# Kernel optimization log

Measured on AMD Instinct MI355X. Metric: run time of the kernel, lower is better.

Reference implementation:

```python
import jax, jax.numpy as jnp
import numpy as np

DIM = 64
NUM_GRAPHS = 256
SLOPE = 11.0 / 48.0  # RReLU eval slope = ((1/8)+(1/3))/2
EPS = 1e-5


def _bn(x, g, b):
    m = x.mean(0)
    v = x.var(0)  # biased, matches torch BN normalization
    return (x - m) * jax.lax.rsqrt(v + EPS) * g + b


def _rrelu(x):
    return jnp.where(x >= 0, x, SLOPE * x)


def _gru(x, h, Wih, Whh, bih, bhh):
    gi = x @ Wih.T + bih
    gh = h @ Whh.T + bhh
    ir, iz, inn = jnp.split(gi, 3, -1)
    hr, hz, hn = jnp.split(gh, 3, -1)
    r = jax.nn.sigmoid(ir + hr)
    z = jax.nn.sigmoid(iz + hz)
    n = jnp.tanh(inn + r * hn)
    return (1.0 - z) * n + z * h


def _nnconv(x, ei, We, bias, n_nodes):
    # edge-conditioned conv: gather src, per-edge matmul, scatter-mean to dst
    src, dst = ei[0], ei[1]
    msg = jnp.einsum('ei,eio->eo', x[src], We)
    s = jax.ops.segment_sum(msg, dst, num_segments=n_nodes)
    cnt = jax.ops.segment_sum(jnp.ones((ei.shape[1],), x.dtype), dst, num_segments=n_nodes)
    return s / jnp.maximum(cnt, 1.0)[:, None] + bias


def _seg_softmax(e, seg, nseg):
    m = jax.ops.segment_max(e, seg, num_segments=nseg)
    ex = jnp.exp(e - m[seg])
    den = jax.ops.segment_sum(ex, seg, num_segments=nseg)
    return ex / den[seg]


def _set2set(x, seg, nseg, Wih, Whh, bih, bhh, steps=3):
    H = x.shape[-1]
    q_star = jnp.zeros((nseg, 2 * H), x.dtype)
    h = jnp.zeros((nseg, H), x.dtype)
    c = jnp.zeros((nseg, H), x.dtype)
    for _ in range(steps):
        gates = q_star @ Wih.T + bih + h @ Whh.T + bhh
        i, f, g, o = jnp.split(gates, 4, -1)
        c = jax.nn.sigmoid(f) * c + jax.nn.sigmoid(i) * jnp.tanh(g)
        h = jax.nn.sigmoid(o) * jnp.tanh(c)
        e = jnp.sum(x * h[seg], -1)
        a = _seg_softmax(e, seg, nseg)
        r = jax.ops.segment_sum(a[:, None] * x, seg, num_segments=nseg)
        q_star = jnp.concatenate([h, r], -1)
    return q_star


def reference(x, edge_index, edge_attr, edge_index3, edge_attr3, batch,
              bnx_g, bnx_b, Wn, bnode, We, be, Wnn1, bias1,
              Wih1, Whh1, bih1, bhh1, bnc_g, bnc_b, Wc1, bc1, Wc2, bc2,
              Wnn2, bias2, Wih2, Whh2, bih2, bhh2,
              Ws_ih, Ws_hh, bs_ih, bs_hh, bno_g, bno_b, Ww, Wb):
    N = x.shape[0]
    out = _rrelu(_bn(x, bnx_g, bnx_b) @ Wn + bnode)          # [N, 64]
    ea = _rrelu(edge_attr @ We + be)                          # [E, 12]
    W1 = (ea @ Wnn1).reshape(-1, DIM, DIM)                    # [E, 64, 64]
    h = out
    for _ in range(2):
        m = _rrelu(_nnconv(out, edge_index, W1, bias1, N))
        h = _gru(m, h, Wih1, Whh1, bih1, bhh1)
        out = h
    out = _bn(out, bnc_g, bnc_b)
    out = _rrelu(out @ Wc1 + bc1)
    out = _rrelu(out @ Wc2 + bc2)                             # [N, 128] (dropout=identity in eval)
    ei3s = jnp.concatenate([edge_index3, edge_index3[::-1]], axis=1)
    ea3s = jnp.concatenate([edge_attr3, edge_attr3], axis=0)
    W2 = (ea3s @ Wnn2).reshape(-1, 2 * DIM, 2 * DIM)          # [2*E3, 128, 128]
    h = out
    for _ in range(2):
        m = _rrelu(_nnconv(out, ei3s, W2, bias2, N))
        h = _gru(m, h, Wih2, Whh2, bih2, bhh2)
        out = h
    cbi = batch[edge_index3[0]]
    pool = _set2set(out, batch, NUM_GRAPHS, Ws_ih, Ws_hh, bs_ih, bs_hh)[cbi]
    t0 = out[edge_index3[0]]
    t1 = out[edge_index3[1]]
    yhat = jnp.concatenate([(t0 + t1) * 0.5, t0 * t1, (t0 - t1) ** 2, pool], axis=1)  # [E3, 640]
    yhat = _bn(yhat, bno_g, bno_b)
    w = edge_attr3 @ Ww
    b = edge_attr3 @ Wb
    return jnp.sum(yhat * w, axis=1) + b[:, 0]


def setup_inputs() -> dict:
    key = jax.random.key(0)
    ks = iter(jax.random.split(key, 64))
    def nrm(shape, scale=1.0):
        return jax.random.normal(next(ks), shape, jnp.float32) * scale
    def lin(i, o):
        return nrm((i, o), 1.0 / np.sqrt(i))
    N, E, E3 = 8192, 16384, 1024
    inp = {}
    inp['x'] = nrm((N, 8))
    inp['edge_index'] = jax.random.randint(next(ks), (2, E), 0, N)
    inp['edge_attr'] = nrm((E, 19))
    inp['edge_index3'] = jax.random.randint(next(ks), (2, E3), 0, N)
    inp['edge_attr3'] = nrm((E3, 8))
    inp['batch'] = jnp.repeat(jnp.arange(NUM_GRAPHS), N // NUM_GRAPHS)
    inp['bnx_g'] = jnp.ones(8); inp['bnx_b'] = jnp.zeros(8)
    inp['Wn'] = lin(8, 64); inp['bnode'] = jnp.zeros(64)
    inp['We'] = lin(19, 12); inp['be'] = jnp.zeros(12)
    inp['Wnn1'] = lin(12, DIM * DIM) * 0.5; inp['bias1'] = jnp.zeros(64)
    inp['Wih1'] = nrm((192, 64), 1.0 / np.sqrt(64)); inp['Whh1'] = nrm((192, 64), 1.0 / np.sqrt(64))
    inp['bih1'] = jnp.zeros(192); inp['bhh1'] = jnp.zeros(192)
    inp['bnc_g'] = jnp.ones(64); inp['bnc_b'] = jnp.zeros(64)
    inp['Wc1'] = lin(64, 128); inp['bc1'] = jnp.zeros(128)
    inp['Wc2'] = lin(128, 128); inp['bc2'] = jnp.zeros(128)
    inp['Wnn2'] = lin(8, 4 * DIM * DIM) * 0.5; inp['bias2'] = jnp.zeros(128)
    inp['Wih2'] = nrm((384, 128), 1.0 / np.sqrt(128)); inp['Whh2'] = nrm((384, 128), 1.0 / np.sqrt(128))
    inp['bih2'] = jnp.zeros(384); inp['bhh2'] = jnp.zeros(384)
    inp['Ws_ih'] = nrm((512, 256), 1.0 / np.sqrt(256)); inp['Ws_hh'] = nrm((512, 128), 1.0 / np.sqrt(128))
    inp['bs_ih'] = jnp.zeros(512); inp['bs_hh'] = jnp.zeros(512)
    inp['bno_g'] = jnp.ones(640); inp['bno_b'] = jnp.zeros(640)
    inp['Ww'] = lin(8, 640); inp['Wb'] = lin(8, 1)
    return inp
```

## Files before the change

kernel.cpp:

```cpp
#include <hip/hip_runtime.h>
#include <hip/hip_bf16.h>
#include <math.h>

#define N_NODES 8192
#define N_EDGES 16384
#define N_E3    1024
#define NGRAPH  256
#define NPG     32
#define SLOPE   (11.0f/48.0f)
#define BN_EPS  1e-5f

__device__ __forceinline__ float rrelu(float v){ return v >= 0.f ? v : SLOPE*v; }
__device__ __forceinline__ float sigm(float v){ return 1.f/(1.f+__expf(-v)); }

typedef _Float16 f16;
typedef __attribute__((ext_vector_type(8))) _Float16 half8v;
typedef __attribute__((ext_vector_type(4))) float f32x4;

template<int PRE, int ACT>
__device__ __forceinline__ void mgemm_body(
    const float* __restrict__ A, const f16* __restrict__ Wh,
    const float* __restrict__ bias,
    const float* __restrict__ q0, const float* __restrict__ q1,
    const float* __restrict__ q2, const float* __restrict__ q3,
    const int* __restrict__ rowidx,
    float* __restrict__ C, int M, int K, int J, int blk) {
  int t = threadIdx.x;
  int lane = t & 63, wv = t >> 6;
  int jt = J >> 6;
  int bm = blk / jt, bj = blk % jt;
  int n0 = (bm << 6) + (wv << 4);
  int j0 = bj << 6;
  int row = n0 + (lane & 15);
  int arow = rowidx ? rowidx[row] : row;
  int kb0 = (lane >> 4) * 8;

  f32x4 acc[4] = {{0.f,0.f,0.f,0.f},{0.f,0.f,0.f,0.f},{0.f,0.f,0.f,0.f},{0.f,0.f,0.f,0.f}};

  float pre_dn = 1.f;
  if (PRE == 1) pre_dn = 1.f / fmaxf(q0[row], 1.f);

  for (int k0 = 0; k0 < K; k0 += 32) {
    int kb = k0 + kb0;
    const float* ap = A + (size_t)arow * K + kb;
    float4 v0 = *(const float4*)ap;
    float4 v1 = *(const float4*)(ap + 4);
    if (PRE == 1) {
      float4 b0 = *(const float4*)(q1 + kb);
      float4 b1 = *(const float4*)(q1 + kb + 4);
      v0.x = rrelu(v0.x*pre_dn + b0.x); v0.y = rrelu(v0.y*pre_dn + b0.y);
      v0.z = rrelu(v0.z*pre_dn + b0.z); v0.w = rrelu(v0.w*pre_dn + b0.w);
      v1.x = rrelu(v1.x*pre_dn + b1.x); v1.y = rrelu(v1.y*pre_dn + b1.y);
      v1.z = rrelu(v1.z*pre_dn + b1.z); v1.w = rrelu(v1.w*pre_dn + b1.w);
    } else if (PRE == 2) {
      float4 m0 = *(const float4*)(q0 + kb), m1 = *(const float4*)(q0 + kb + 4);
      float4 s0 = *(const float4*)(q1 + kb), s1 = *(const float4*)(q1 + kb + 4);
      float4 g0 = *(const float4*)(q2 + kb), g1 = *(const float4*)(q2 + kb + 4);
      float4 h0 = *(const float4*)(q3 + kb), h1 = *(const float4*)(q3 + kb + 4);
      v0.x = (v0.x-m0.x)*rsqrtf(s0.x+BN_EPS)*g0.x + h0.x;
      v0.y = (v0.y-m0.y)*rsqrtf(s0.y+BN_EPS)*g0.y + h0.y;
      v0.z = (v0.z-m0.z)*rsqrtf(s0.z+BN_EPS)*g0.z + h0.z;
      v0.w = (v0.w-m0.w)*rsqrtf(s0.w+BN_EPS)*g0.w + h0.w;
      v1.x = (v1.x-m1.x)*rsqrtf(s1.x+BN_EPS)*g1.x + h1.x;
      v1.y = (v1.y-m1.y)*rsqrtf(s1.y+BN_EPS)*g1.y + h1.y;
      v1.z = (v1.z-m1.z)*rsqrtf(s1.z+BN_EPS)*g1.z + h1.z;
      v1.w = (v1.w-m1.w)*rsqrtf(s1.w+BN_EPS)*g1.w + h1.w;
    }
    half8v af;
    af[0]=(f16)v0.x; af[1]=(f16)v0.y; af[2]=(f16)v0.z; af[3]=(f16)v0.w;
    af[4]=(f16)v1.x; af[5]=(f16)v1.y; af[6]=(f16)v1.z; af[7]=(f16)v1.w;
    #pragma unroll
    for (int jf = 0; jf < 4; jf++) {
      const f16* wp = Wh + (size_t)(j0 + jf*16 + (lane & 15)) * K + kb;
      half8v wf = *(const half8v*)wp;
      acc[jf] = __builtin_amdgcn_mfma_f32_16x16x32_f16(af, wf, acc[jf], 0, 0, 0);
    }
  }
  int r0 = (bm << 6) + (wv << 4) + ((lane >> 4) << 2);
  #pragma unroll
  for (int jf = 0; jf < 4; jf++) {
    int col = j0 + jf*16 + (lane & 15);
    float bv = bias ? bias[col] : 0.f;
    #pragma unroll
    for (int r = 0; r < 4; r++) {
      float o = acc[jf][r] + bv;
      if (ACT == 1) o = rrelu(o);
      C[(size_t)(r0 + r) * J + col] = o;
    }
  }
}

template<int PRE, int ACT>
__global__ __launch_bounds__(256) void mgemm_k(
    const float* __restrict__ A, const f16* __restrict__ Wh, const float* __restrict__ bias,
    const float* __restrict__ q0, const float* __restrict__ q1,
    const float* __restrict__ q2, const float* __restrict__ q3,
    const int* __restrict__ rowidx,
    float* __restrict__ C, int M, int K, int J,
    int nblk, float* __restrict__ zptr, int zcount) {
  int blk = blockIdx.x;
  if (blk >= nblk) {
    int zb = blk - nblk;
    float4 z4 = make_float4(0.f,0.f,0.f,0.f);
    for (int i = zb*256 + (int)threadIdx.x; i*4 < zcount; i += 16*256)
      ((float4*)zptr)[i] = z4;
    return;
  }
  mgemm_body<PRE,ACT>(A, Wh, bias, q0, q1, q2, q3, rowidx, C, M, K, J, blk);
}

template<int LOGH>
__global__ void gruf_k(const float* __restrict__ sbuf, const float* __restrict__ cnt,
                       const float* __restrict__ mbias,
                       const f16* __restrict__ Wih, const f16* __restrict__ Whh,
                       const float* __restrict__ bih, const float* __restrict__ bhh,
                       const float* __restrict__ hold, float* __restrict__ hnew) {
  const int H = 1 << LOGH;
  const int K = H;
  const int jt = H >> 6;
  int t = threadIdx.x;
  int lane = t & 63, wv = t >> 6;
  int wpb = blockDim.x >> 6;
  int bm = blockIdx.x / jt, bj = blockIdx.x % jt;
  int n0 = bm * (wpb << 4) + (wv << 4);
  int j0 = bj << 6;
  int row = n0 + (lane & 15);
  int kb0 = (lane >> 4) * 8;

  f32x4 aR[4]  = {{0.f,0.f,0.f,0.f},{0.f,0.f,0.f,0.f},{0.f,0.f,0.f,0.f},{0.f,0.f,0.f,0.f}};
  f32x4 aZ[4]  = {{0.f,0.f,0.f,0.f},{0.f,0.f,0.f,0.f},{0.f,0.f,0.f,0.f},{0.f,0.f,0.f,0.f}};
  f32x4 aIN[4] = {{0.f,0.f,0.f,0.f},{0.f,0.f,0.f,0.f},{0.f,0.f,0.f,0.f},{0.f,0.f,0.f,0.f}};
  f32x4 aHN[4] = {{0.f,0.f,0.f,0.f},{0.f,0.f,0.f,0.f},{0.f,0.f,0.f,0.f},{0.f,0.f,0.f,0.f}};

  float dn = 1.f / fmaxf(cnt[row], 1.f);
  for (int k0 = 0; k0 < K; k0 += 32) {
    int kb = k0 + kb0;
    const float* ap = sbuf + (size_t)row * K + kb;
    float4 v0 = *(const float4*)ap, v1 = *(const float4*)(ap + 4);
    float4 b0 = *(const float4*)(mbias + kb), b1 = *(const float4*)(mbias + kb + 4);
    half8v af;
    af[0]=(f16)rrelu(v0.x*dn+b0.x); af[1]=(f16)rrelu(v0.y*dn+b0.y);
    af[2]=(f16)rrelu(v0.z*dn+b0.z); af[3]=(f16)rrelu(v0.w*dn+b0.w);
    af[4]=(f16)rrelu(v1.x*dn+b1.x); af[5]=(f16)rrelu(v1.y*dn+b1.y);
    af[6]=(f16)rrelu(v1.z*dn+b1.z); af[7]=(f16)rrelu(v1.w*dn+b1.w);
    #pragma unroll
    for (int jf = 0; jf < 4; jf++) {
      int wr = j0 + jf*16 + (lane & 15);
      half8v wR = *(const half8v*)(Wih + (size_t)wr*K + kb);
      half8v wZ = *(const half8v*)(Wih + (size_t)(H + wr)*K + kb);
      half8v wN = *(const half8v*)(Wih + (size_t)(2*H + wr)*K + kb);
      aR[jf]  = __builtin_amdgcn_mfma_f32_16x16x32_f16(af, wR, aR[jf], 0, 0, 0);
      aZ[jf]  = __builtin_amdgcn_mfma_f32_16x16x32_f16(af, wZ, aZ[jf], 0, 0, 0);
      aIN[jf] = __builtin_amdgcn_mfma_f32_16x16x32_f16(af, wN, aIN[jf], 0, 0, 0);
    }
  }
  for (int k0 = 0; k0 < K; k0 += 32) {
    int kb = k0 + kb0;
    const float* ap = hold + (size_t)row * K + kb;
    float4 v0 = *(const float4*)ap, v1 = *(const float4*)(ap + 4);
    half8v af;
    af[0]=(f16)v0.x; af[1]=(f16)v0.y; af[2]=(f16)v0.z; af[3]=(f16)v0.w;
    af[4]=(f16)v1.x; af[5]=(f16)v1.y; af[6]=(f16)v1.z; af[7]=(f16)v1.w;
    #pragma unroll
    for (int jf = 0; jf < 4; jf++) {
      int wr = j0 + jf*16 + (lane & 15);
      half8v wR = *(const half8v*)(Whh + (size_t)wr*K + kb);
      half8v wZ = *(const half8v*)(Whh + (size_t)(H + wr)*K + kb);
      half8v wN = *(const half8v*)(Whh + (size_t)(2*H + wr)*K + kb);
      aR[jf]  = __builtin_amdgcn_mfma_f32_16x16x32_f16(af, wR, aR[jf], 0, 0, 0);
      aZ[jf]  = __builtin_amdgcn_mfma_f32_16x16x32_f16(af, wZ, aZ[jf], 0, 0, 0);
      aHN[jf] = __builtin_amdgcn_mfma_f32_16x16x32_f16(af, wN, aHN[jf], 0, 0, 0);
    }
  }
  int r0 = n0 + ((lane >> 4) << 2);
  #pragma unroll
  for (int jf = 0; jf < 4; jf++) {
    int col = j0 + jf*16 + (lane & 15);
    float bR = bih[col] + bhh[col];
    float bZ = bih[H + col] + bhh[H + col];
    float bI = bih[2*H + col], bH = bhh[2*H + col];
    #pragma unroll
    for (int r = 0; r < 4; r++) {
      float rr = sigm(aR[jf][r] + bR);
      float zz = sigm(aZ[jf][r] + bZ);
      float nn = tanhf(aIN[jf][r] + bI + rr*(aHN[jf][r] + bH));
      float ho = hold[(size_t)(r0 + r)*H + col];
      hnew[(size_t)(r0 + r)*H + col] = (1.f - zz)*nn + zz*ho;
    }
  }
}

__global__ void bn_stats_k(const float* __restrict__ X, int nrow, int F,
                           float* __restrict__ mean, float* __restrict__ var) {
  int f = blockIdx.x, t = threadIdx.x;
  __shared__ float s1[256], s2[256];
  float a = 0.f, b = 0.f;
  for (int n = t; n < nrow; n += 256) {
    float v = X[(size_t)n * F + f];
    a += v; b += v * v;
  }
  s1[t] = a; s2[t] = b; __syncthreads();
  for (int w = 128; w > 0; w >>= 1) {
    if (t < w) { s1[t] += s1[t+w]; s2[t] += s2[t+w]; }
    __syncthreads();
  }
  if (t == 0) {
    float m = s1[0] / (float)nrow;
    mean[f] = m;
    var[f]  = s2[0] / (float)nrow - m * m;
  }
}

__global__ void embed_k(const float* __restrict__ x,
                        const float* __restrict__ mean, const float* __restrict__ var,
                        const float* __restrict__ g, const float* __restrict__ b,
                        const float* __restrict__ Wn, const float* __restrict__ bnode,
                        float* __restrict__ nodeA,
                        const float* __restrict__ eattr,
                        const float* __restrict__ We, const float* __restrict__ be,
                        float* __restrict__ ea12) {
  if (blockIdx.x < 2048) {
    int idx = blockIdx.x * 256 + threadIdx.x;
    int n = idx >> 6, o = idx & 63;
    float acc = bnode[o];
    #pragma unroll
    for (int i = 0; i < 8; i++) {
      float xn = (x[n*8+i] - mean[i]) * rsqrtf(var[i] + BN_EPS) * g[i] + b[i];
      acc += xn * Wn[i*64 + o];
    }
    nodeA[idx] = rrelu(acc);
  } else {
    int idx = (blockIdx.x - 2048) * 256 + threadIdx.x;
    if (idx >= N_EDGES * 12) return;
    int e = idx / 12, j = idx - e * 12;
    float acc = be[j];
    #pragma unroll
    for (int k = 0; k < 19; k++) acc += eattr[e*19+k] * We[k*12 + j];
    ea12[idx] = rrelu(acc);
  }
}

__global__ void pack_k(const float* __restrict__ Wnn1,
                       const float* __restrict__ Wih1, const float* __restrict__ Whh1,
                       const float* __restrict__ Wc1,  const float* __restrict__ Wc2,
                       const float* __restrict__ Wnn2,
                       const float* __restrict__ Wih2, const float* __restrict__ Whh2,
                       const float* __restrict__ Ws_ih, const float* __restrict__ Ws_hh,
                       f16* __restrict__ Wz1h,
                       f16* __restrict__ Wih1h, f16* __restrict__ Whh1h,
                       f16* __restrict__ Wc1Th, f16* __restrict__ Wc2Th,
                       f16* __restrict__ W2fh,
                       f16* __restrict__ Wih2h, f16* __restrict__ Whh2h,
                       float* __restrict__ Wfold,
                       float* __restrict__ cnt1, float* __restrict__ cnt2) {
  int idx = blockIdx.x * 256 + threadIdx.x;
  if (idx < 49152) {
    int jj = idx >> 6, i = idx & 63;
    int k = jj >> 6, o = jj & 63;
    Wz1h[idx] = (f16)Wnn1[k*4096 + i*64 + o];
  }
  if (idx < 12288) { Wih1h[idx] = (f16)Wih1[idx]; Whh1h[idx] = (f16)Whh1[idx]; }
  if (idx < 8192) {
    int o = idx >> 6, i = idx & 63;
    Wc1Th[idx] = (f16)Wc1[i*128 + o];
  }
  if (idx < 16384) {
    int o = idx >> 7, i = idx & 127;
    Wc2Th[idx] = (f16)Wc2[i*128 + o];
  }
  if (idx < 131072) {
    int r = idx >> 7, i = idx & 127;
    int k = r >> 7, o = r & 127;
    W2fh[idx] = (f16)Wnn2[k*16384 + i*128 + o];
  }
  if (idx < 49152) { Wih2h[idx] = (f16)Wih2[idx]; Whh2h[idx] = (f16)Whh2[idx]; }
  if (idx < 131072) {
    int i = idx >> 9, j = idx & 511;
    float v = Ws_ih[(size_t)j*256 + i];
    if (i < 128) v += Ws_hh[(size_t)j*128 + i];
    Wfold[idx] = v;
  }
  if (idx < N_NODES) { cnt1[idx] = 0.f; cnt2[idx] = 0.f; }
}

__global__ void cnt_k(const int* __restrict__ ei, const int* __restrict__ ei3,
                      float* __restrict__ cnt1, float* __restrict__ cnt2) {
  int idx = blockIdx.x * 256 + threadIdx.x;
  if (idx < N_EDGES) atomicAdd(&cnt1[ei[N_EDGES + idx]], 1.0f);
  if (idx < N_E3) {
    atomicAdd(&cnt2[ei3[N_E3 + idx]], 1.0f);
    atomicAdd(&cnt2[ei3[idx]], 1.0f);
  }
}

__global__ void conv1_msg_k(const float* __restrict__ Z, const int* __restrict__ ei,
                            const float* __restrict__ ea, float* __restrict__ sbuf) {
  int idx = blockIdx.x * 256 + threadIdx.x;
  if (idx >= N_EDGES * 64) return;
  int e = idx >> 6, o = idx & 63;
  int src = ei[e], dst = ei[N_EDGES + e];
  const float* z = Z + (size_t)src * 768 + o;
  float msg = 0.f;
  #pragma unroll
  for (int k = 0; k < 12; k++) msg += ea[e*12 + k] * z[k*64];
  atomicAdd(&sbuf[dst*64 + o], msg);
}

__global__ void conv2_msg_k(const float* __restrict__ Zg, const int* __restrict__ ei3,
                            const float* __restrict__ ea3, float* __restrict__ sbuf) {
  int idx = blockIdx.x * 256 + threadIdx.x;
  if (idx >= 2*N_E3*128) return;
  int e = idx >> 7, o = idx & 127;
  int eb = e & (N_E3 - 1);
  int dst = ei3[(e + N_E3) & (2*N_E3 - 1)];
  const float* z = Zg + (size_t)e*1024 + o;
  float msg = 0.f;
  #pragma unroll
  for (int k = 0; k < 8; k++) msg += ea3[eb*8 + k] * z[k*128];
  atomicAdd(&sbuf[dst*128 + o], msg);
}

__global__ __launch_bounds__(1024) void set2set_k(const float* __restrict__ x,
    const float* __restrict__ Wfold,
    const float* __restrict__ bs_ih, const float* __restrict__ bs_hh,
    float* __restrict__ qpool) {
  int g = blockIdx.x, t = threadIdx.x;
  __shared__ float xs[NPG*128];
  __shared__ float hr[256];
  __shared__ float cbuf[128];
  __shared__ float pbuf[1024];
  __shared__ float abuf[NPG];
  *(float4*)&xs[t*4] = *(const float4*)(x + (size_t)g*NPG*128 + t*4);
  if (t < 128) {
    float gi = bs_ih[t]     + bs_hh[t];
    float gg = bs_ih[256+t] + bs_hh[256+t];
    float go = bs_ih[384+t] + bs_hh[384+t];
    float c0 = sigm(gi) * tanhf(gg);
    cbuf[t] = c0;
    hr[t] = sigm(go) * tanhf(c0);
  }
  __syncthreads();
  #pragma unroll 1
  for (int step = 0; step < 3; step++) {
    {
      int node = t >> 5, s = t & 31;
      const float* xr = xs + node*128 + s*4;
      float p = xr[0]*hr[s*4] + xr[1]*hr[s*4+1] + xr[2]*hr[s*4+2] + xr[3]*hr[s*4+3];
      p += __shfl_down(p, 16, 32); p += __shfl_down(p, 8, 32);
      p += __shfl_down(p, 4, 32);  p += __shfl_down(p, 2, 32);
      p += __shfl_down(p, 1, 32);
      if (s == 0) pbuf[node] = p;
    }
    __syncthreads();
    if (t < NPG) {
      float e = pbuf[t];
      float mx = e;
      for (int o = 16; o > 0; o >>= 1) mx = fmaxf(mx, __shfl_xor(mx, o, 32));
      float ex = __expf(e - mx);
      float den = ex;
      for (int o = 16; o > 0; o >>= 1) den += __shfl_xor(den, o, 32);
      abuf[t] = ex / den;
    }
    __syncthreads();
    if (t < 128) {
      float r = 0.f;
      #pragma unroll 8
      for (int nn = 0; nn < NPG; nn++) r += abuf[nn] * xs[nn*128 + t];
      hr[128 + t] = r;
    }
    __syncthreads();
    if (step == 2) break;
    {
      int j = t & 511, half = t >> 9;
      const float* wp = Wfold + (size_t)(half*128)*512 + j;
      const float* iv = hr + half*128;
      float a0=0.f, a1=0.f, a2=0.f, a3=0.f;
      #pragma unroll 4
      for (int i = 0; i < 128; i += 4) {
        a0 += iv[i]   * wp[(i)  *512];
        a1 += iv[i+1] * wp[(i+1)*512];
        a2 += iv[i+2] * wp[(i+2)*512];
        a3 += iv[i+3] * wp[(i+3)*512];
      }
      pbuf[t] = a0 + a1 + a2 + a3;
    }
    __syncthreads();
    if (t < 128) {
      float gi = pbuf[t]     + pbuf[512+t] + bs_ih[t]     + bs_hh[t];
      float gf = pbuf[128+t] + pbuf[640+t] + bs_ih[128+t] + bs_hh[128+t];
      float gg = pbuf[256+t] + pbuf[768+t] + bs_ih[256+t] + bs_hh[256+t];
      float go = pbuf[384+t] + pbuf[896+t] + bs_ih[384+t] + bs_hh[384+t];
      float ci = sigm(gf) * cbuf[t] + sigm(gi) * tanhf(gg);
      cbuf[t] = ci;
      hr[t] = sigm(go) * tanhf(ci);
    }
    __syncthreads();
  }
  if (t < 256) qpool[g*256 + t] = hr[t];
}

__global__ void yhat_k(const float* __restrict__ feat, const int* __restrict__ ei3,
                       const int* __restrict__ batch, const float* __restrict__ qpool,
                       float* __restrict__ yhat) {
  int idx = blockIdx.x * blockDim.x + threadIdx.x;
  if (idx >= N_E3 * 640) return;
  int e = idx / 640, j = idx - e * 640;
  int s0 = ei3[e], s1 = ei3[N_E3 + e];
  float v;
  if (j < 128)      { v = 0.5f * (feat[s0*128+j] + feat[s1*128+j]); }
  else if (j < 256) { int jj = j-128; v = feat[s0*128+jj] * feat[s1*128+jj]; }
  else if (j < 384) { int jj = j-256; float d = feat[s0*128+jj] - feat[s1*128+jj]; v = d*d; }
  else              { int cbi = batch[s0]; v = qpool[cbi*256 + (j-384)]; }
  yhat[idx] = v;
}

__global__ void final_k(const float* __restrict__ yhat,
                        const float* __restrict__ mean, const float* __restrict__ var,
                        const float* __restrict__ g, const float* __restrict__ b,
                        const float* __restrict__ ea3,
                        const float* __restrict__ Ww, const float* __restrict__ Wb,
                        float* __restrict__ out) {
  int e = blockIdx.x, t = threadIdx.x;
  __shared__ float red[128];
  float av[8];
  #pragma unroll
  for (int k = 0; k < 8; k++) av[k] = ea3[e*8 + k];
  float acc = 0.f;
  for (int j = t; j < 640; j += 128) {
    float yn = (yhat[(size_t)e*640 + j] - mean[j]) * rsqrtf(var[j] + BN_EPS) * g[j] + b[j];
    float wj = 0.f;
    #pragma unroll
    for (int k = 0; k < 8; k++) wj += av[k] * Ww[k*640 + j];
    acc += yn * wj;
  }
  red[t] = acc; __syncthreads();
  for (int w = 64; w > 0; w >>= 1) {
    if (t < w) red[t] += red[t+w];
    __syncthreads();
  }
  if (t == 0) {
    float bb = 0.f;
    #pragma unroll
    for (int k = 0; k < 8; k++) bb += av[k] * Wb[k];
    out[e] = red[0] + bb;
  }
}

extern "C" void kernel_launch(void* const* d_in, const int* in_sizes, int n_in,
                              void* d_out, int out_size, void* d_ws, size_t ws_size,
                              hipStream_t stream) {
  const float* x      = (const float*)d_in[0];
  const int*   ei     = (const int*)  d_in[1];
  const float* eattr  = (const float*)d_in[2];
  const int*   ei3    = (const int*)  d_in[3];
  const float* ea3    = (const float*)d_in[4];
  const int*   batch  = (const int*)  d_in[5];
  const float* bnx_g  = (const float*)d_in[6];
  const float* bnx_b  = (const float*)d_in[7];
  const float* Wn     = (const float*)d_in[8];
  const float* bnode  = (const float*)d_in[9];
  const float* We     = (const float*)d_in[10];
  const float* be     = (const float*)d_in[11];
  const float* Wnn1   = (const float*)d_in[12];
  const float* bias1  = (const float*)d_in[13];
  const float* Wih1   = (const float*)d_in[14];
  const float* Whh1   = (const float*)d_in[15];
  const float* bih1   = (const float*)d_in[16];
  const float* bhh1   = (const float*)d_in[17];
  const float* bnc_g  = (const float*)d_in[18];
  const float* bnc_b  = (const float*)d_in[19];
  const float* Wc1    = (const float*)d_in[20];
  const float* bc1    = (const float*)d_in[21];
  const float* Wc2    = (const float*)d_in[22];
  const float* bc2    = (const float*)d_in[23];
  const float* Wnn2   = (const float*)d_in[24];
  const float* bias2  = (const float*)d_in[25];
  const float* Wih2   = (const float*)d_in[26];
  const float* Whh2   = (const float*)d_in[27];
  const float* bih2   = (const float*)d_in[28];
  const float* bhh2   = (const float*)d_in[29];
  const float* Ws_ih  = (const float*)d_in[30];
  const float* Ws_hh  = (const float*)d_in[31];
  const float* bs_ih  = (const float*)d_in[32];
  const float* bs_hh  = (const float*)d_in[33];
  const float* bno_g  = (const float*)d_in[34];
  const float* bno_b  = (const float*)d_in[35];
  const float* Ww     = (const float*)d_in[36];
  const float* Wb     = (const float*)d_in[37];
  float* out = (float*)d_out;

  float* W = (float*)d_ws;
  size_t off = 0;
  float* Wfold  = W + off; off += 131072;
  float* ea12   = W + off; off += (size_t)N_EDGES * 12;
  float* nodeA  = W + off; off += (size_t)N_NODES * 64;
  float* nodeA2 = W + off; off += (size_t)N_NODES * 64;
  float* sbuf   = W + off; off += (size_t)N_NODES * 128;
  float* cnt1   = W + off; off += (size_t)N_NODES;
  float* cnt2   = W + off; off += (size_t)N_NODES;
  float* y1     = W + off; off += (size_t)N_NODES * 128;
  float* nodeB  = W + off; off += (size_t)N_NODES * 128;
  float* nodeB2 = W + off; off += (size_t)N_NODES * 128;
  float* Z      = W + off; off += (size_t)N_NODES * 768;
  float* qpool  = W + off; off += (size_t)NGRAPH * 256;
  float* yhat   = W + off; off += (size_t)N_E3 * 640;
  float* mean   = W + off; off += 640;
  float* var    = W + off; off += 640;
  f16* F = (f16*)(W + off);
  size_t foff = 0;
  f16* Wz1h  = F + foff; foff += 49152;
  f16* Wih1h = F + foff; foff += 12288;
  f16* Whh1h = F + foff; foff += 12288;
  f16* Wc1Th = F + foff; foff += 8192;
  f16* Wc2Th = F + foff; foff += 16384;
  f16* W2fh  = F + foff; foff += 131072;
  f16* Wih2h = F + foff; foff += 49152;
  f16* Whh2h = F + foff; foff += 49152;
  (void)foff; (void)ws_size; (void)in_sizes; (void)n_in; (void)out_size;

  float* Zg = Z;

  pack_k<<<512, 256, 0, stream>>>(Wnn1, Wih1, Whh1, Wc1, Wc2, Wnn2, Wih2, Whh2, Ws_ih, Ws_hh,
                                  Wz1h, Wih1h, Whh1h, Wc1Th, Wc2Th, W2fh, Wih2h, Whh2h,
                                  Wfold, cnt1, cnt2);
  cnt_k<<<(N_EDGES+255)/256, 256, 0, stream>>>(ei, ei3, cnt1, cnt2);

  bn_stats_k<<<8, 256, 0, stream>>>(x, N_NODES, 8, mean, var);
  embed_k<<<2048 + 768, 256, 0, stream>>>(x, mean, var, bnx_g, bnx_b, Wn, bnode, nodeA,
                                          eattr, We, be, ea12);

  {
    float* s0 = nodeA; float* s1 = nodeA2;
    for (int it = 0; it < 2; it++) {
      mgemm_k<0,0><<<1536 + 16, 256, 0, stream>>>(s0, Wz1h, nullptr,
          nullptr, nullptr, nullptr, nullptr, nullptr, Z, N_NODES, 64, 768,
          1536, sbuf, N_NODES*64);
      conv1_msg_k<<<(N_EDGES*64)/256, 256, 0, stream>>>(Z, ei, ea12, sbuf);
      gruf_k<6><<<256, 128, 0, stream>>>(sbuf, cnt1, bias1, Wih1h, Whh1h, bih1, bhh1, s0, s1);
      float* tmp = s0; s0 = s1; s1 = tmp;
    }
  }

  bn_stats_k<<<64, 256, 0, stream>>>(nodeA, N_NODES, 64, mean, var);
  mgemm_k<2,1><<<256, 256, 0, stream>>>(nodeA, Wc1Th, bc1,
      mean, var, bnc_g, bnc_b, nullptr, y1, N_NODES, 64, 128, 256, nullptr, 0);
  mgemm_k<0,1><<<256, 256, 0, stream>>>(y1, Wc2Th, bc2,
      nullptr, nullptr, nullptr, nullptr, nullptr, nodeB, N_NODES, 128, 128, 256, nullptr, 0);

  {
    float* s0 = nodeB; float* s1 = nodeB2;
    for (int it = 0; it < 2; it++) {
      mgemm_k<0,0><<<512 + 16, 256, 0, stream>>>(s0, W2fh, nullptr,
          nullptr, nullptr, nullptr, nullptr, ei3, Zg, 2*N_E3, 128, 1024,
          512, sbuf, N_NODES*128);
      conv2_msg_k<<<(2*N_E3*128)/256, 256, 0, stream>>>(Zg, ei3, ea3, sbuf);
      gruf_k<7><<<256, 256, 0, stream>>>(sbuf, cnt2, bias2, Wih2h, Whh2h, bih2, bhh2, s0, s1);
      float* tmp = s0; s0 = s1; s1 = tmp;
    }
  }

  set2set_k<<<NGRAPH, 1024, 0, stream>>>(nodeB, Wfold, bs_ih, bs_hh, qpool);

  yhat_k<<<(N_E3*640 + 255)/256, 256, 0, stream>>>(nodeB, ei3, batch, qpool, yhat);
  bn_stats_k<<<640, 256, 0, stream>>>(yhat, N_E3, 640, mean, var);
  final_k<<<N_E3, 128, 0, stream>>>(yhat, mean, var, bno_g, bno_b, ea3, Ww, Wb, out);
}
```

Baseline: 232.7 us.

## Fuse edge-conditioned conv GEMMs into per-edge MFMA kernels and merge small launches

Replaces the node-level Z precompute GEMM plus the separate message kernel with per-edge kernels. These gather source features, scale them by the edge attributes, run MFMA against the reshaped edge weights and scatter results to destinations atomically, so the large Z intermediate is never materialised. Count accumulation and buffer zeroing move into the embed and GRU kernels. BatchNorm statistics are accumulated in the GRU epilogue, and the two FC layers become one kernel that keeps the intermediate in shared memory. In exchange, the conv1 per-edge recompute is larger than the node-level GEMM, and register pressure and atomic traffic rise.

New measurement: 273.4 us. +17.5%, slower.

```diff
diff --git a/kernel.cpp b/kernel.cpp
--- a/kernel.cpp
+++ b/kernel.cpp
@@ -17,104 +17,121 @@
 typedef __attribute__((ext_vector_type(8))) _Float16 half8v;
 typedef __attribute__((ext_vector_type(4))) float f32x4;
 
-template<int PRE, int ACT>
-__device__ __forceinline__ void mgemm_body(
-    const float* __restrict__ A, const f16* __restrict__ Wh,
-    const float* __restrict__ bias,
-    const float* __restrict__ q0, const float* __restrict__ q1,
-    const float* __restrict__ q2, const float* __restrict__ q3,
-    const int* __restrict__ rowidx,
-    float* __restrict__ C, int M, int K, int J, int blk) {
-  int t = threadIdx.x;
-  int lane = t & 63, wv = t >> 6;
-  int jt = J >> 6;
-  int bm = blk / jt, bj = blk % jt;
-  int n0 = (bm << 6) + (wv << 4);
-  int j0 = bj << 6;
-  int row = n0 + (lane & 15);
-  int arow = rowidx ? rowidx[row] : row;
+__device__ __forceinline__ void zero_tail(int zb, float* zptr, int zcount) {
+  float4 z4 = make_float4(0.f,0.f,0.f,0.f);
+  int bd = blockDim.x;
+  for (int i = zb*bd + (int)threadIdx.x; i*4 < zcount; i += 16*bd)
+    ((float4*)zptr)[i] = z4;
+}
+
+__global__ __launch_bounds__(256) void conv1f_k(const float* __restrict__ nodeA,
+    const int* __restrict__ ei, const float* __restrict__ ea,
+    const f16* __restrict__ Wz1h, float* __restrict__ sbuf) {
+  int t = threadIdx.x, lane = t & 63, wv = t >> 6;
+  int e0 = blockIdx.x*64 + wv*16;
+  int eA = e0 + (lane & 15);
+  int src = ei[eA];
   int kb0 = (lane >> 4) * 8;
-
-  f32x4 acc[4] = {{0.f,0.f,0.f,0.f},{0.f,0.f,0.f,0.f},{0.f,0.f,0.f,0.f},{0.f,0.f,0.f,0.f}};
-
-  float pre_dn = 1.f;
-  if (PRE == 1) pre_dn = 1.f / fmaxf(q0[row], 1.f);
-
-  for (int k0 = 0; k0 < K; k0 += 32) {
-    int kb = k0 + kb0;
-    const float* ap = A + (size_t)arow * K + kb;
-    float4 v0 = *(const float4*)ap;
-    float4 v1 = *(const float4*)(ap + 4);
-    if (PRE == 1) {
-      float4 b0 = *(const float4*)(q1 + kb);
-      float4 b1 = *(const float4*)(q1 + kb + 4);
-      v0.x = rrelu(v0.x*pre_dn + b0.x); v0.y = rrelu(v0.y*pre_dn + b0.y);
-      v0.z = rrelu(v0.z*pre_dn + b0.z); v0.w = rrelu(v0.w*pre_dn + b0.w);
-      v1.x = rrelu(v1.x*pre_dn + b1.x); v1.y = rrelu(v1.y*pre_dn + b1.y);
-      v1.z = rrelu(v1.z*pre_dn + b1.z); v1.w = rrelu(v1.w*pre_dn + b1.w);
-    } else if (PRE == 2) {
-      float4 m0 = *(const float4*)(q0 + kb), m1 = *(const float4*)(q0 + kb + 4);
-      float4 s0 = *(const float4*)(q1 + kb), s1 = *(const float4*)(q1 + kb + 4);
-      float4 g0 = *(const float4*)(q2 + kb), g1 = *(const float4*)(q2 + kb + 4);
-      float4 h0 = *(const float4*)(q3 + kb), h1 = *(const float4*)(q3 + kb + 4);
-      v0.x = (v0.x-m0.x)*rsqrtf(s0.x+BN_EPS)*g0.x + h0.x;
-      v0.y = (v0.y-m0.y)*rsqrtf(s0.y+BN_EPS)*g0.y + h0.y;
-      v0.z = (v0.z-m0.z)*rsqrtf(s0.z+BN_EPS)*g0.z + h0.z;
-      v0.w = (v0.w-m0.w)*rsqrtf(s0.w+BN_EPS)*g0.w + h0.w;
-      v1.x = (v1.x-m1.x)*rsqrtf(s1.x+BN_EPS)*g1.x + h1.x;
-      v1.y = (v1.y-m1.y)*rsqrtf(s1.y+BN_EPS)*g1.y + h1.y;
-      v1.z = (v1.z-m1.z)*rsqrtf(s1.z+BN_EPS)*g1.z + h1.z;
-      v1.w = (v1.w-m1.w)*rsqrtf(s1.w+BN_EPS)*g1.w + h1.w;
-    }
-    half8v af;
-    af[0]=(f16)v0.x; af[1]=(f16)v0.y; af[2]=(f16)v0.z; af[3]=(f16)v0.w;
-    af[4]=(f16)v1.x; af[5]=(f16)v1.y; af[6]=(f16)v1.z; af[7]=(f16)v1.w;
+  const float* ap = nodeA + (size_t)src*64 + kb0;
+  float4 v0 = *(const float4*)ap,      v1 = *(const float4*)(ap+4);
+  float4 v2 = *(const float4*)(ap+32), v3 = *(const float4*)(ap+36);
+  half8v a0, a1;
+  a0[0]=(f16)v0.x; a0[1]=(f16)v0.y; a0[2]=(f16)v0.z; a0[3]=(f16)v0.w;
+  a0[4]=(f16)v1.x; a0[5]=(f16)v1.y; a0[6]=(f16)v1.z; a0[7]=(f16)v1.w;
+  a1[0]=(f16)v2.x; a1[1]=(f16)v2.y; a1[2]=(f16)v2.z; a1[3]=(f16)v2.w;
+  a1[4]=(f16)v3.x; a1[5]=(f16)v3.y; a1[6]=(f16)v3.z; a1[7]=(f16)v3.w;
+  float eav[12];
+  #pragma unroll
+  for (int kg = 0; kg < 12; kg++) eav[kg] = ea[eA*12 + kg];
+
+  f32x4 acc[4] = {{0,0,0,0},{0,0,0,0},{0,0,0,0},{0,0,0,0}};
+  #pragma unroll
+  for (int kg = 0; kg < 12; kg++) {
+    f16 s = (f16)eav[kg];
+    half8v s0, s1;
+    #pragma unroll
+    for (int u = 0; u < 8; u++) { s0[u] = a0[u]*s; s1[u] = a1[u]*s; }
     #pragma unroll
     for (int jf = 0; jf < 4; jf++) {
-      const f16* wp = Wh + (size_t)(j0 + jf*16 + (lane & 15)) * K + kb;
-      half8v wf = *(const half8v*)wp;
-      acc[jf] = __builtin_amdgcn_mfma_f32_16x16x32_f16(af, wf, acc[jf], 0, 0, 0);
-    }
-  }
-  int r0 = (bm << 6) + (wv << 4) + ((lane >> 4) << 2);
+      const f16* wp = Wz1h + (size_t)(kg*64 + jf*16 + (lane & 15))*64 + kb0;
+      acc[jf] = __builtin_amdgcn_mfma_f32_16x16x32_f16(s0, *(const half8v*)wp, acc[jf], 0, 0, 0);
+      acc[jf] = __builtin_amdgcn_mfma_f32_16x16x32_f16(s1, *(const half8v*)(wp+32), acc[jf], 0, 0, 0);
+    }
+  }
+  int dstv[4];
+  #pragma unroll
+  for (int r = 0; r < 4; r++) dstv[r] = ei[N_EDGES + e0 + ((lane>>4)<<2) + r];
   #pragma unroll
   for (int jf = 0; jf < 4; jf++) {
-    int col = j0 + jf*16 + (lane & 15);
-    float bv = bias ? bias[col] : 0.f;
-    #pragma unroll
-    for (int r = 0; r < 4; r++) {
-      float o = acc[jf][r] + bv;
-      if (ACT == 1) o = rrelu(o);
-      C[(size_t)(r0 + r) * J + col] = o;
-    }
-  }
-}
-
-template<int PRE, int ACT>
-__global__ __launch_bounds__(256) void mgemm_k(
-    const float* __restrict__ A, const f16* __restrict__ Wh, const float* __restrict__ bias,
-    const float* __restrict__ q0, const float* __restrict__ q1,
-    const float* __restrict__ q2, const float* __restrict__ q3,
-    const int* __restrict__ rowidx,
-    float* __restrict__ C, int M, int K, int J,
-    int nblk, float* __restrict__ zptr, int zcount) {
-  int blk = blockIdx.x;
-  if (blk >= nblk) {
-    int zb = blk - nblk;
-    float4 z4 = make_float4(0.f,0.f,0.f,0.f);
-    for (int i = zb*256 + (int)threadIdx.x; i*4 < zcount; i += 16*256)
-      ((float4*)zptr)[i] = z4;
-    return;
-  }
-  mgemm_body<PRE,ACT>(A, Wh, bias, q0, q1, q2, q3, rowidx, C, M, K, J, blk);
-}
-
-template<int LOGH>
+    int col = jf*16 + (lane & 15);
+    #pragma unroll
+    for (int r = 0; r < 4; r++)
+      atomicAdd(&sbuf[dstv[r]*64 + col], acc[jf][r]);
+  }
+}
+
+__global__ __launch_bounds__(256) void conv2f_k(const float* __restrict__ nodeB,
+    const int* __restrict__ ei3, const float* __restrict__ ea3,
+    const f16* __restrict__ W2fh, float* __restrict__ sbuf) {
+  int t = threadIdx.x, lane = t & 63, wv = t >> 6;
+  int e0 = blockIdx.x*64 + wv*16;
+  int eA = e0 + (lane & 15);
+  int src = ei3[eA];
+  int kb0 = (lane >> 4) * 8;
+  const float* ap = nodeB + (size_t)src*128 + kb0;
+  half8v a[4];
+  #pragma unroll
+  for (int kg = 0; kg < 4; kg++) {
+    float4 w0 = *(const float4*)(ap + kg*32);
+    float4 w1 = *(const float4*)(ap + kg*32 + 4);
+    a[kg][0]=(f16)w0.x; a[kg][1]=(f16)w0.y; a[kg][2]=(f16)w0.z; a[kg][3]=(f16)w0.w;
+    a[kg][4]=(f16)w1.x; a[kg][5]=(f16)w1.y; a[kg][6]=(f16)w1.z; a[kg][7]=(f16)w1.w;
+  }
+  int eb = eA & (N_E3 - 1);
+  float eav[8];
+  #pragma unroll
+  for (int kg = 0; kg < 8; kg++) eav[kg] = ea3[eb*8 + kg];
+
+  f32x4 acc[8] = {{0,0,0,0},{0,0,0,0},{0,0,0,0},{0,0,0,0},
+                  {0,0,0,0},{0,0,0,0},{0,0,0,0},{0,0,0,0}};
+  #pragma unroll 1
+  for (int kg = 0; kg < 8; kg++) {
+    f16 s = (f16)eav[kg];
+    half8v sa[4];
+    #pragma unroll
+    for (int q = 0; q < 4; q++) {
+      #pragma unroll
+      for (int u = 0; u < 8; u++) sa[q][u] = a[q][u]*s;
+    }
+    #pragma unroll
+    for (int jf = 0; jf < 8; jf++) {
+      const f16* wp = W2fh + (size_t)(kg*128 + jf*16 + (lane & 15))*128 + kb0;
+      #pragma unroll
+      for (int q = 0; q < 4; q++)
+        acc[jf] = __builtin_amdgcn_mfma_f32_16x16x32_f16(sa[q], *(const half8v*)(wp + q*32), acc[jf], 0, 0, 0);
+    }
+  }
+  int dstv[4];
+  #pragma unroll
+  for (int r = 0; r < 4; r++) dstv[r] = ei3[(e0 + ((lane>>4)<<2) + r + N_E3) & (2*N_E3 - 1)];
+  #pragma unroll
+  for (int jf = 0; jf < 8; jf++) {
+    int col = jf*16 + (lane & 15);
+    #pragma unroll
+    for (int r = 0; r < 4; r++)
+      atomicAdd(&sbuf[dstv[r]*128 + col], acc[jf][r]);
+  }
+}
+
+template<int LOGH, int STATS>
 __global__ void gruf_k(const float* __restrict__ sbuf, const float* __restrict__ cnt,
                        const float* __restrict__ mbias,
                        const f16* __restrict__ Wih, const f16* __restrict__ Whh,
                        const float* __restrict__ bih, const float* __restrict__ bhh,
-                       const float* __restrict__ hold, float* __restrict__ hnew) {
+                       const float* __restrict__ hold, float* __restrict__ hnew,
+                       float* __restrict__ bns1, float* __restrict__ bns2,
+                       int nblk, float* __restrict__ zptr, int zcount) {
+  if ((int)blockIdx.x >= nblk) { zero_tail(blockIdx.x - nblk, zptr, zcount); return; }
   const int H = 1 << LOGH;
   const int K = H;
   const int jt = H >> 6;
@@ -127,12 +144,12 @@
   int row = n0 + (lane & 15);
   int kb0 = (lane >> 4) * 8;
 
-  f32x4 aR[4]  = {{0.f,0.f,0.f,0.f},{0.f,0.f,0.f,0.f},{0.f,0.f,0.f,0.f},{0.f,0.f,0.f,0.f}};
-  f32x4 aZ[4]  = {{0.f,0.f,0.f,0.f},{0.f,0.f,0.f,0.f},{0.f,0.f,0.f,0.f},{0.f,0.f,0.f,0.f}};
-  f32x4 aIN[4] = {{0.f,0.f,0.f,0.f},{0.f,0.f,0.f,0.f},{0.f,0.f,0.f,0.f},{0.f,0.f,0.f,0.f}};
-  f32x4 aHN[4] = {{0.f,0.f,0.f,0.f},{0.f,0.f,0.f,0.f},{0.f,0.f,0.f,0.f},{0.f,0.f,0.f,0.f}};
-
-  float dn = 1.f / fmaxf(cnt[row], 1.f);
+  f32x4 aR[4]  = {{0,0,0,0},{0,0,0,0},{0,0,0,0},{0,0,0,0}};
+  f32x4 aZ[4]  = {{0,0,0,0},{0,0,0,0},{0,0,0,0},{0,0,0,0}};
+  f32x4 aIN[4] = {{0,0,0,0},{0,0,0,0},{0,0,0,0},{0,0,0,0}};
+  f32x4 aHN[4] = {{0,0,0,0},{0,0,0,0},{0,0,0,0},{0,0,0,0}};
+
+  float dn = 1.f / fmaxf(cnt[row], 1.0f);
   for (int k0 = 0; k0 < K; k0 += 32) {
     int kb = k0 + kb0;
     const float* ap = sbuf + (size_t)row * K + kb;
@@ -179,14 +196,90 @@
     float bR = bih[col] + bhh[col];
     float bZ = bih[H + col] + bhh[H + col];
     float bI = bih[2*H + col], bH = bhh[2*H + col];
+    float ssum = 0.f, sq = 0.f;
     #pragma unroll
     for (int r = 0; r < 4; r++) {
       float rr = sigm(aR[jf][r] + bR);
       float zz = sigm(aZ[jf][r] + bZ);
       float nn = tanhf(aIN[jf][r] + bI + rr*(aHN[jf][r] + bH));
       float ho = hold[(size_t)(r0 + r)*H + col];
-      hnew[(size_t)(r0 + r)*H + col] = (1.f - zz)*nn + zz*ho;
-    }
+      float hv = (1.f - zz)*nn + zz*ho;
+      hnew[(size_t)(r0 + r)*H + col] = hv;
+      if (STATS) { ssum += hv; sq += hv*hv; }
+    }
+    if (STATS) {
+      ssum += __shfl_xor(ssum, 16); ssum += __shfl_xor(ssum, 32);
+      sq   += __shfl_xor(sq, 16);   sq   += __shfl_xor(sq, 32);
+      if (lane < 16) { atomicAdd(&bns1[col], ssum); atomicAdd(&bns2[col], sq); }
+    }
+  }
+}
+
+__global__ __launch_bounds__(256) void fcf_k(const float* __restrict__ A,
+    const f16* __restrict__ W1, const float* __restrict__ b1v,
+    const f16* __restrict__ W2, const float* __restrict__ b2v,
+    const float* __restrict__ bns1, const float* __restrict__ bns2,
+    const float* __restrict__ g, const float* __restrict__ b,
+    float* __restrict__ outB,
+    int nblk, float* __restrict__ zptr, int zcount) {
+  if ((int)blockIdx.x >= nblk) { zero_tail(blockIdx.x - nblk, zptr, zcount); return; }
+  __shared__ f16 y1s[4][16][128];
+  int t = threadIdx.x, lane = t & 63, wv = t >> 6;
+  int n0 = blockIdx.x*64 + wv*16;
+  int row = n0 + (lane & 15);
+  int kb0 = (lane >> 4) * 8;
+  const float invN = 1.f / (float)N_NODES;
+
+  const float* ap = A + (size_t)row*64 + kb0;
+  half8v af0, af1;
+  #pragma unroll
+  for (int u = 0; u < 8; u++) {
+    int k0i = kb0 + u, k1i = 32 + kb0 + u;
+    float m0 = bns1[k0i]*invN, m1 = bns1[k1i]*invN;
+    float va0 = bns2[k0i]*invN - m0*m0, va1 = bns2[k1i]*invN - m1*m1;
+    af0[u] = (f16)((ap[u]    - m0)*rsqrtf(va0+BN_EPS)*g[k0i] + b[k0i]);
+    af1[u] = (f16)((ap[32+u] - m1)*rsqrtf(va1+BN_EPS)*g[k1i] + b[k1i]);
+  }
+  f32x4 acc1[8] = {{0,0,0,0},{0,0,0,0},{0,0,0,0},{0,0,0,0},
+                   {0,0,0,0},{0,0,0,0},{0,0,0,0},{0,0,0,0}};
+  #pragma unroll
+  for (int jf = 0; jf < 8; jf++) {
+    const f16* wp = W1 + (size_t)(jf*16 + (lane & 15))*64 + kb0;
+    acc1[jf] = __builtin_amdgcn_mfma_f32_16x16x32_f16(af0, *(const half8v*)wp, acc1[jf], 0, 0, 0);
+    acc1[jf] = __builtin_amdgcn_mfma_f32_16x16x32_f16(af1, *(const half8v*)(wp+32), acc1[jf], 0, 0, 0);
+  }
+  #pragma unroll
+  for (int jf = 0; jf < 8; jf++) {
+    int col = jf*16 + (lane & 15);
+    float bv = b1v[col];
+    #pragma unroll
+    for (int r = 0; r < 4; r++) {
+      int rl = ((lane >> 4) << 2) + r;
+      y1s[wv][rl][col] = (f16)rrelu(acc1[jf][r] + bv);
+    }
+  }
+  __syncthreads();
+  half8v bf[4];
+  #pragma unroll
+  for (int q = 0; q < 4; q++)
+    bf[q] = *(const half8v*)&y1s[wv][lane & 15][q*32 + kb0];
+  f32x4 acc2[8] = {{0,0,0,0},{0,0,0,0},{0,0,0,0},{0,0,0,0},
+                   {0,0,0,0},{0,0,0,0},{0,0,0,0},{0,0,0,0}};
+  #pragma unroll
+  for (int jf = 0; jf < 8; jf++) {
+    const f16* wp = W2 + (size_t)(jf*16 + (lane & 15))*128 + kb0;
+    #pragma unroll
+    for (int q = 0; q < 4; q++)
+      acc2[jf] = __builtin_amdgcn_mfma_f32_16x16x32_f16(bf[q], *(const half8v*)(wp + q*32), acc2[jf], 0, 0, 0);
+  }
+  int r0 = n0 + ((lane >> 4) << 2);
+  #pragma unroll
+  for (int jf = 0; jf < 8; jf++) {
+    int col = jf*16 + (lane & 15);
+    float bv = b2v[col];
+    #pragma unroll
+    for (int r = 0; r < 4; r++)
+      outB[(size_t)(r0 + r)*128 + col] = rrelu(acc2[jf][r] + bv);
   }
 }
 
@@ -218,9 +311,13 @@
                         float* __restrict__ nodeA,
                         const float* __restrict__ eattr,
                         const float* __restrict__ We, const float* __restrict__ be,
-                        float* __restrict__ ea12) {
-  if (blockIdx.x < 2048) {
-    int idx = blockIdx.x * 256 + threadIdx.x;
+                        float* __restrict__ ea12,
+                        const int* __restrict__ ei, const int* __restrict__ ei3,
+                        float* __restrict__ cnt1, float* __restrict__ cnt2,
+                        float* __restrict__ zptr) {
+  int bid = blockIdx.x, t = threadIdx.x;
+  if (bid < 2048) {
+    int idx = bid * 256 + t;
     int n = idx >> 6, o = idx & 63;
     float acc = bnode[o];
     #pragma unroll
@@ -229,14 +326,23 @@
       acc += xn * Wn[i*64 + o];
     }
     nodeA[idx] = rrelu(acc);
-  } else {
-    int idx = (blockIdx.x - 2048) * 256 + threadIdx.x;
+  } else if (bid < 2816) {
+    int idx = (bid - 2048) * 256 + t;
     if (idx >= N_EDGES * 12) return;
     int e = idx / 12, j = idx - e * 12;
     float acc = be[j];
     #pragma unroll
     for (int k = 0; k < 19; k++) acc += eattr[e*19+k] * We[k*12 + j];
     ea12[idx] = rrelu(acc);
+  } else if (bid < 2880) {
+    int idx = (bid - 2816) * 256 + t;
+    if (idx < N_EDGES) atomicAdd(&cnt1[ei[N_EDGES + idx]], 1.0f);
+    if (idx < N_E3) {
+      atomicAdd(&cnt2[ei3[N_E3 + idx]], 1.0f);
+      atomicAdd(&cnt2[ei3[idx]], 1.0f);
+    }
+  } else {
+    zero_tail(bid - 2880, zptr, N_NODES*64);
   }
 }
 
@@ -252,7 +358,8 @@
                        f16* __restrict__ W2fh,
                        f16* __restrict__ Wih2h, f16* __restrict__ Whh2h,
                        float* __restrict__ Wfold,
-                       float* __restrict__ cnt1, float* __restrict__ cnt2) {
+                       float* __restrict__ cnt1, float* __restrict__ cnt2,
+                       float* __restrict__ bns1, float* __restrict__ bns2) {
   int idx = blockIdx.x * 256 + threadIdx.x;
   if (idx < 49152) {
     int jj = idx >> 6, i = idx & 63;
@@ -281,43 +388,7 @@
     Wfold[idx] = v;
   }
   if (idx < N_NODES) { cnt1[idx] = 0.f; cnt2[idx] = 0.f; }
-}
-
-__global__ void cnt_k(const int* __restrict__ ei, const int* __restrict__ ei3,
-                      float* __restrict__ cnt1, float* __restrict__ cnt2) {
-  int idx = blockIdx.x * 256 + threadIdx.x;
-  if (idx < N_EDGES) atomicAdd(&cnt1[ei[N_EDGES + idx]], 1.0f);
-  if (idx < N_E3) {
-    atomicAdd(&cnt2[ei3[N_E3 + idx]], 1.0f);
-    atomicAdd(&cnt2[ei3[idx]], 1.0f);
-  }
-}
-
-__global__ void conv1_msg_k(const float* __restrict__ Z, const int* __restrict__ ei,
-                            const float* __restrict__ ea, float* __restrict__ sbuf) {
-  int idx = blockIdx.x * 256 + threadIdx.x;
-  if (idx >= N_EDGES * 64) return;
-  int e = idx >> 6, o = idx & 63;
-  int src = ei[e], dst = ei[N_EDGES + e];
-  const float* z = Z + (size_t)src * 768 + o;
-  float msg = 0.f;
-  #pragma unroll
-  for (int k = 0; k < 12; k++) msg += ea[e*12 + k] * z[k*64];
-  atomicAdd(&sbuf[dst*64 + o], msg);
-}
-
-__global__ void conv2_msg_k(const float* __restrict__ Zg, const int* __restrict__ ei3,
-                            const float* __restrict__ ea3, float* __restrict__ sbuf) {
-  int idx = blockIdx.x * 256 + threadIdx.x;
-  if (idx >= 2*N_E3*128) return;
-  int e = idx >> 7, o = idx & 127;
-  int eb = e & (N_E3 - 1);
-  int dst = ei3[(e + N_E3) & (2*N_E3 - 1)];
-  const float* z = Zg + (size_t)e*1024 + o;
-  float msg = 0.f;
-  #pragma unroll
-  for (int k = 0; k < 8; k++) msg += ea3[eb*8 + k] * z[k*128];
-  atomicAdd(&sbuf[dst*128 + o], msg);
+  if (idx < 128) { bns1[idx] = 0.f; bns2[idx] = 0.f; }
 }
 
 __global__ __launch_bounds__(1024) void set2set_k(const float* __restrict__ x,
@@ -495,17 +566,20 @@
   float* ea12   = W + off; off += (size_t)N_EDGES * 12;
   float* nodeA  = W + off; off += (size_t)N_NODES * 64;
   float* nodeA2 = W + off; off += (size_t)N_NODES * 64;
-  float* sbuf   = W + off; off += (size_t)N_NODES * 128;
+  float* sA1    = W + off; off += (size_t)N_NODES * 64;
+  float* sA2    = W + off; off += (size_t)N_NODES * 64;
+  float* sB1    = W + off; off += (size_t)N_NODES * 128;
+  float* sB2    = W + off; off += (size_t)N_NODES * 128;
   float* cnt1   = W + off; off += (size_t)N_NODES;
   float* cnt2   = W + off; off += (size_t)N_NODES;
-  float* y1     = W + off; off += (size_t)N_NODES * 128;
   float* nodeB  = W + off; off += (size_t)N_NODES * 128;
   float* nodeB2 = W + off; off += (size_t)N_NODES * 128;
-  float* Z      = W + off; off += (size_t)N_NODES * 768;
   float* qpool  = W + off; off += (size_t)NGRAPH * 256;
   float* yhat   = W + off; off += (size_t)N_E3 * 640;
   float* mean   = W + off; off += 640;
   float* var    = W + off; off += 640;
+  float* bns1   = W + off; off += 128;
+  float* bns2   = W + off; off += 128;
   f16* F = (f16*)(W + off);
   size_t foff = 0;
   f16* Wz1h  = F + foff; foff += 49152;
@@ -518,46 +592,34 @@
   f16* Whh2h = F + foff; foff += 49152;
   (void)foff; (void)ws_size; (void)in_sizes; (void)n_in; (void)out_size;
 
-  float* Zg = Z;
-
   pack_k<<<512, 256, 0, stream>>>(Wnn1, Wih1, Whh1, Wc1, Wc2, Wnn2, Wih2, Whh2, Ws_ih, Ws_hh,
                                   Wz1h, Wih1h, Whh1h, Wc1Th, Wc2Th, W2fh, Wih2h, Whh2h,
-                                  Wfold, cnt1, cnt2);
-  cnt_k<<<(N_EDGES+255)/256, 256, 0, stream>>>(ei, ei3, cnt1, cnt2);
-
+                                  Wfold, cnt1, cnt2, bns1, bns2);
   bn_stats_k<<<8, 256, 0, stream>>>(x, N_NODES, 8, mean, var);
-  embed_k<<<2048 + 768, 256, 0, stream>>>(x, mean, var, bnx_g, bnx_b, Wn, bnode, nodeA,
-                                          eattr, We, be, ea12);
-
-  {
-    float* s0 = nodeA; float* s1 = nodeA2;
-    for (int it = 0; it < 2; it++) {
-      mgemm_k<0,0><<<1536 + 16, 256, 0, stream>>>(s0, Wz1h, nullptr,
-          nullptr, nullptr, nullptr, nullptr, nullptr, Z, N_NODES, 64, 768,
-          1536, sbuf, N_NODES*64);
-      conv1_msg_k<<<(N_EDGES*64)/256, 256, 0, stream>>>(Z, ei, ea12, sbuf);
-      gruf_k<6><<<256, 128, 0, stream>>>(sbuf, cnt1, bias1, Wih1h, Whh1h, bih1, bhh1, s0, s1);
-      float* tmp = s0; s0 = s1; s1 = tmp;
-    }
-  }
-
-  bn_stats_k<<<64, 256, 0, stream>>>(nodeA, N_NODES, 64, mean, var);
-  mgemm_k<2,1><<<256, 256, 0, stream>>>(nodeA, Wc1Th, bc1,
-      mean, var, bnc_g, bnc_b, nullptr, y1, N_NODES, 64, 128, 256, nullptr, 0);
-  mgemm_k<0,1><<<256, 256, 0, stream>>>(y1, Wc2Th, bc2,
-      nullptr, nullptr, nullptr, nullptr, nullptr, nodeB, N_NODES, 128, 128, 256, nullptr, 0);
-
-  {
-    float* s0 = nodeB; float* s1 = nodeB2;
-    for (int it = 0; it < 2; it++) {
-      mgemm_k<0,0><<<512 + 16, 256, 0, stream>>>(s0, W2fh, nullptr,
-          nullptr, nullptr, nullptr, nullptr, ei3, Zg, 2*N_E3, 128, 1024,
-          512, sbuf, N_NODES*128);
-      conv2_msg_k<<<(2*N_E3*128)/256, 256, 0, stream>>>(Zg, ei3, ea3, sbuf);
-      gruf_k<7><<<256, 256, 0, stream>>>(sbuf, cnt2, bias2, Wih2h, Whh2h, bih2, bhh2, s0, s1);
-      float* tmp = s0; s0 = s1; s1 = tmp;
-    }
-  }
+  embed_k<<<2896, 256, 0, stream>>>(x, mean, var, bnx_g, bnx_b, Wn, bnode, nodeA,
+                                    eattr, We, be, ea12, ei, ei3, cnt1, cnt2, sA1);
+
+  conv1f_k<<<256, 256, 0, stream>>>(nodeA, ei, ea12, Wz1h, sA1);
+  gruf_k<6,0><<<272, 128, 0, stream>>>(sA1, cnt1, bias1, Wih1h, Whh1h, bih1, bhh1,
+                                       nodeA, nodeA2, nullptr, nullptr,
+                                       256, sA2, N_NODES*64);
+  conv1f_k<<<256, 256, 0, stream>>>(nodeA2, ei, ea12, Wz1h, sA2);
+  gruf_k<6,1><<<272, 128, 0, stream>>>(sA2, cnt1, bias1, Wih1h, Whh1h, bih1, bhh1,
+                                       nodeA2, nodeA, bns1, bns2,
+                                       256, sB1, N_NODES*128);
+
+  fcf_k<<<144, 256, 0, stream>>>(nodeA, Wc1Th, bc1, Wc2Th, bc2,
+                                 bns1, bns2, bnc_g, bnc_b, nodeB,
+                                 128, sB2, N_NODES*128);
+
+  conv2f_k<<<32, 256, 0, stream>>>(nodeB, ei3, ea3, W2fh, sB1);
+  gruf_k<7,0><<<256, 256, 0, stream>>>(sB1, cnt2, bias2, Wih2h, Whh2h, bih2, bhh2,
+                                       nodeB, nodeB2, nullptr, nullptr,
+                                       256, nullptr, 0);
+  conv2f_k<<<32, 256, 0, stream>>>(nodeB2, ei3, ea3, W2fh, sB2);
+  gruf_k<7,0><<<256, 256, 0, stream>>>(sB2, cnt2, bias2, Wih2h, Whh2h, bih2, bhh2,
+                                       nodeB2, nodeB, nullptr, nullptr,
+                                       256, nullptr, 0);
 
   set2set_k<<<NGRAPH, 1024, 0, stream>>>(nodeB, Wfold, bs_ih, bs_hh, qpool);
 
```
